# Optimization experiments

Measured on AMD Instinct MI355X. Metric: run time of the kernel, lower is better.

Reference implementation:

```python
import jax, jax.numpy as jnp
import numpy as np

B, NX, NY = 4, 128, 128
DIM, DH, HEADS, LATENT, DOUT = 128, 64, 8, 64, 128
KM = 3
KD = DH * KM          # per-head low-rank-kernel dim (192)
SCALING = 1.0         # kernel_multiplier<=4 and softmax=False -> scaling_factor
ROT_SCALE = 64.0      # 1/min_freq of continuous RotaryEmbedding (min_freq=1/64)
EPS = 1e-5


def layer_norm(x, g, b):
    m = x.mean(-1, keepdims=True)
    v = jnp.var(x, axis=-1, keepdims=True)
    return (x - m) * jax.lax.rsqrt(v + EPS) * g + b


def pooling_reducer(x, Win, g, b, W1, b1, W2, b2):
    # x: [b, n, m, c] -> mean over axis 2 -> PreNorm(MLP with gated GELU) -> [b, n, latent]
    h = (x @ Win).mean(axis=2)
    h = layer_norm(h, g, b)
    h = h @ W1 + b1
    c = h.shape[-1] // 2
    h = jax.nn.gelu(h[..., :c], approximate=False) * h[..., c:]
    return h @ W2 + b2


def rotary(t, pos):
    # t: [b,h,n,d], pos: [n] continuous coordinates
    d = t.shape[-1]
    inv_freq = 1.0 / (10000.0 ** (jnp.arange(0, d, 2, dtype=jnp.float32) / d))
    f = (pos * ROT_SCALE)[:, None] * inv_freq          # [n, d//2]
    f = jnp.concatenate([f, f], axis=-1)               # [n, d]
    cos, sin = jnp.cos(f), jnp.sin(f)
    x1, x2 = jnp.split(t, 2, axis=-1)
    rot = jnp.concatenate([-x2, x1], axis=-1)          # rotate_half (half-split variant)
    return t * cos + rot * sin


def low_rank_kernel(u, pos, Wqk):
    # u: [b, n, latent] -> kernel K: [b, h, n, n]
    b, n, _ = u.shape
    qk = u @ Wqk                                       # [b, n, 2*h*KD]
    q, k = jnp.split(qk, 2, axis=-1)
    q = q.reshape(b, n, HEADS, KD).transpose(0, 2, 1, 3)
    k = k.reshape(b, n, HEADS, KD).transpose(0, 2, 1, 3)
    q = rotary(q, pos)
    k = rotary(k, pos)
    return jnp.einsum('bhid,bhjd->bhij', q, k) * SCALING


def setup_inputs():
    key = jax.random.key(0)
    ks = jax.random.split(key, 16)
    s = 0.02
    def rn(k, shape):
        return jax.random.normal(k, shape, dtype=jnp.float32) * s
    return {
        'u': jax.random.normal(ks[0], (B, NX, NY, DIM), dtype=jnp.float32),
        'pos_x': jnp.sort(jax.random.uniform(ks[1], (NX,), dtype=jnp.float32)),
        'pos_y': jnp.sort(jax.random.uniform(ks[2], (NY,), dtype=jnp.float32)),
        'ln_g': jnp.ones((DIM,), jnp.float32),
        'ln_b': jnp.zeros((DIM,), jnp.float32),
        'Wv': rn(ks[3], (DIM, HEADS * DH)),
        'Win': rn(ks[4], (DIM, DIM)),
        'px_Win': rn(ks[5], (DIM, DIM)),
        'px_g': jnp.ones((DIM,), jnp.float32),
        'px_b': jnp.zeros((DIM,), jnp.float32),
        'px_W1': rn(ks[6], (DIM, 2 * DIM)),
        'px_b1': jnp.zeros((2 * DIM,), jnp.float32),
        'px_W2': rn(ks[7], (DIM, LATENT)),
        'px_b2': jnp.zeros((LATENT,), jnp.float32),
        'py_Win': rn(ks[8], (DIM, DIM)),
        'py_g': jnp.ones((DIM,), jnp.float32),
        'py_b': jnp.zeros((DIM,), jnp.float32),
        'py_W1': rn(ks[9], (DIM, 2 * DIM)),
        'py_b1': jnp.zeros((2 * DIM,), jnp.float32),
        'py_W2': rn(ks[10], (DIM, LATENT)),
        'py_b2': jnp.zeros((LATENT,), jnp.float32),
        'Wqk_x': rn(ks[11], (LATENT, 2 * HEADS * KD)),
        'Wqk_y': rn(ks[12], (LATENT, 2 * HEADS * KD)),
        'Wo1': rn(ks[13], (HEADS * DH, DOUT)),
        'Wo2': rn(ks[14], (DOUT, DOUT)),
    }


def reference(u, pos_x, pos_y, ln_g, ln_b, Wv, Win,
              px_Win, px_g, px_b, px_W1, px_b1, px_W2, px_b2,
              py_Win, py_g, py_b, py_W1, py_b1, py_W2, py_b2,
              Wqk_x, Wqk_y, Wo1, Wo2):
    un = layer_norm(u, ln_g, ln_b)                      # [b,nx,ny,dim]
    v = un @ Wv                                         # [b,nx,ny,h*dh]
    ui = un @ Win
    ux = pooling_reducer(ui, px_Win, px_g, px_b, px_W1, px_b1, px_W2, px_b2)                       # [b,nx,L]
    uy = pooling_reducer(ui.transpose(0, 2, 1, 3), py_Win, py_g, py_b, py_W1, py_b1, py_W2, py_b2)  # [b,ny,L]
    kx = low_rank_kernel(ux, pos_x, Wqk_x)              # [b,h,nx,nx]
    ky = low_rank_kernel(uy, pos_y, Wqk_y)              # [b,h,ny,ny]
    b, nx, ny, _ = u.shape
    vphi = v.reshape(b, nx, ny, HEADS, DH).transpose(0, 3, 1, 2, 4)   # b h i l c
    t = jnp.einsum('bhij,bhjmc->bhimc', kx, vphi)       # attend along x axis
    t = jnp.einsum('bhlm,bhimc->bhilc', ky, t)          # attend along y axis
    t = t.transpose(0, 2, 3, 1, 4).reshape(b, nx, ny, HEADS * DH)
    # InstanceNorm2d applied to a channels-LAST tensor (as in the original repo):
    # torch treats dim1 (nx) as channels, normalizing over (ny, h*dh) per (b, nx), no affine.
    m = t.mean(axis=(2, 3), keepdims=True)
    var = t.var(axis=(2, 3), keepdims=True)
    t = (t - m) * jax.lax.rsqrt(var + EPS)
    h = jax.nn.gelu(t @ Wo1, approximate=False)
    return h @ Wo2
```

## Files before the change

kernel.cpp:

```cpp
#include <hip/hip_runtime.h>
#include <math.h>

#define ROWS 65536
#define KDD 192

typedef __attribute__((ext_vector_type(8))) short bfrag;
typedef __attribute__((ext_vector_type(4))) float facc;

__device__ inline unsigned short bf16r(float x) {
  union { float f; unsigned u; } v; v.f = x;
  unsigned r = v.u + 0x7fffu + ((v.u >> 16) & 1u);
  return (unsigned short)(r >> 16);
}
__device__ inline float bf2f(unsigned short h) {
  union { unsigned u; float f; } v; v.u = ((unsigned)h) << 16; return v.f;
}
__device__ inline float gelu_f(float x) {
  return x * 0.5f * (1.f + erff(x * 0.70710678f));
}

__global__ __launch_bounds__(128) void k_ln(const float* __restrict__ x,
                                            const float* __restrict__ g,
                                            const float* __restrict__ bb,
                                            unsigned short* __restrict__ y) {
  int row = blockIdx.x;
  int t = threadIdx.x;
  float v = x[(size_t)row * 128 + t];
  float s = v, s2 = v * v;
  for (int off = 32; off > 0; off >>= 1) {
    s += __shfl_down(s, off, 64);
    s2 += __shfl_down(s2, off, 64);
  }
  __shared__ float ps[2], ps2[2];
  int wid = t >> 6, lane = t & 63;
  if (lane == 0) { ps[wid] = s; ps2[wid] = s2; }
  __syncthreads();
  float S = ps[0] + ps[1], S2 = ps2[0] + ps2[1];
  float mean = S * (1.f / 128.f);
  float var = S2 * (1.f / 128.f) - mean * mean;
  float r = rsqrtf(var + 1e-5f);
  y[(size_t)row * 128 + t] = bf16r((v - mean) * r * g[t] + bb[t]);
}

__global__ __launch_bounds__(128) void k_means(const unsigned short* __restrict__ un,
                                               float* __restrict__ mx, float* __restrict__ my) {
  int blk = blockIdx.x;
  int c = threadIdx.x;
  if (blk < 512) {
    const unsigned short* p = un + (size_t)blk * 16384 + c;
    float s = 0;
    for (int j = 0; j < 128; j++) s += bf2f(p[(size_t)j * 128]);
    mx[(size_t)blk * 128 + c] = s * (1.f / 128.f);
  } else {
    int bj = blk - 512;
    int b = bj >> 7, j = bj & 127;
    const unsigned short* p = un + (size_t)b * 2097152 + (size_t)j * 128 + c;
    float s = 0;
    for (int i = 0; i < 128; i++) s += bf2f(p[(size_t)i * 16384]);
    my[(size_t)bj * 128 + c] = s * (1.f / 128.f);
  }
}

__global__ __launch_bounds__(256) void k_wprep(const float* __restrict__ Wv,
                                               const float* __restrict__ Wo1,
                                               const float* __restrict__ Wo2,
                                               unsigned short* __restrict__ WvT,
                                               unsigned short* __restrict__ Wo1T,
                                               unsigned short* __restrict__ Wo2T,
                                               float* __restrict__ scol) {
  int blk = blockIdx.x, t = threadIdx.x;
  if (blk < 256) {
    int idx = blk * 256 + t;
    int c = idx >> 7, r = idx & 127;
    WvT[(size_t)c * 128 + r] = bf16r(Wv[(size_t)r * 512 + c]);
  } else if (blk < 512) {
    int idx = (blk - 256) * 256 + t;
    int n = idx >> 9, k = idx & 511;
    Wo1T[(size_t)n * 512 + k] = bf16r(Wo1[(size_t)k * 128 + n]);
  } else if (blk < 576) {
    int idx = (blk - 512) * 256 + t;
    int n = idx >> 7, k = idx & 127;
    Wo2T[n * 128 + k] = bf16r(Wo2[k * 128 + n]);
  } else {
    if (t < 128) {
      float a = 0;
      for (int k = 0; k < 512; k++) a += bf2f(bf16r(Wo1[k * 128 + t]));
      scol[t] = a;
    }
  }
}

__global__ __launch_bounds__(256) void k_gemmz(const float* __restrict__ A0,
                                               const float* __restrict__ B0,
                                               float* __restrict__ C0,
                                               const float* __restrict__ A1,
                                               const float* __restrict__ B1,
                                               float* __restrict__ C1,
                                               int K, int lda, int ldb, int ldc) {
  const float* A = blockIdx.z ? A1 : A0;
  const float* Bm = blockIdx.z ? B1 : B0;
  float* C = blockIdx.z ? C1 : C0;
  __shared__ float As[16][64];
  __shared__ float Bs[16][64];
  int tid = threadIdx.x;
  int n0 = blockIdx.x * 64, m0 = blockIdx.y * 64;
  int tx = tid & 15, ty = tid >> 4;
  float acc[4][4] = {};
  int la_m = tid >> 2, la_k = (tid & 3) * 4;
  int lb_k = tid >> 4, lb_n = (tid & 15) * 4;
  for (int k0 = 0; k0 < K; k0 += 16) {
    float4 a4 = *(const float4*)(A + (size_t)(m0 + la_m) * lda + k0 + la_k);
    As[la_k + 0][la_m] = a4.x; As[la_k + 1][la_m] = a4.y;
    As[la_k + 2][la_m] = a4.z; As[la_k + 3][la_m] = a4.w;
    float4 b4 = *(const float4*)(Bm + (size_t)(k0 + lb_k) * ldb + n0 + lb_n);
    *(float4*)&Bs[lb_k][lb_n] = b4;
    __syncthreads();
#pragma unroll
    for (int kk = 0; kk < 16; kk++) {
      float4 av = *(const float4*)&As[kk][ty * 4];
      float4 bv = *(const float4*)&Bs[kk][tx * 4];
      float a[4] = {av.x, av.y, av.z, av.w};
      float b[4] = {bv.x, bv.y, bv.z, bv.w};
#pragma unroll
      for (int i = 0; i < 4; i++)
#pragma unroll
        for (int j = 0; j < 4; j++) acc[i][j] += a[i] * b[j];
    }
    __syncthreads();
  }
#pragma unroll
  for (int i = 0; i < 4; i++) {
    float4 o;
    o.x = acc[i][0]; o.y = acc[i][1]; o.z = acc[i][2]; o.w = acc[i][3];
    *(float4*)(C + (size_t)(m0 + ty * 4 + i) * ldc + n0 + tx * 4) = o;
  }
}

__global__ __launch_bounds__(128) void k_pool2(const float* __restrict__ in0, const float* __restrict__ in1,
                                               const float* __restrict__ Wc0, const float* __restrict__ Wc1,
                                               const float* __restrict__ g0, const float* __restrict__ g1,
                                               const float* __restrict__ bb0, const float* __restrict__ bb1,
                                               const float* __restrict__ W10, const float* __restrict__ W11,
                                               const float* __restrict__ b10, const float* __restrict__ b11,
                                               const float* __restrict__ W20, const float* __restrict__ W21,
                                               const float* __restrict__ b20, const float* __restrict__ b21,
                                               float* __restrict__ o0, float* __restrict__ o1) {
  int sel = blockIdx.y;
  const float* in = sel ? in1 : in0;  const float* Wc = sel ? Wc1 : Wc0;
  const float* g = sel ? g1 : g0;     const float* bb = sel ? bb1 : bb0;
  const float* W1 = sel ? W11 : W10;  const float* b1 = sel ? b11 : b10;
  const float* W2 = sel ? W21 : W20;  const float* b2 = sel ? b21 : b20;
  float* out = sel ? o1 : o0;
  int row = blockIdx.x;
  int t = threadIdx.x;
  __shared__ float xin[128], h1[128], h3[128];
  __shared__ float ps[2], ps2[2];
  xin[t] = in[(size_t)row * 128 + t];
  __syncthreads();
  float a = 0;
  for (int k = 0; k < 128; k++) a += xin[k] * Wc[k * 128 + t];
  float s = a, s2 = a * a;
  for (int off = 32; off > 0; off >>= 1) {
    s += __shfl_down(s, off, 64);
    s2 += __shfl_down(s2, off, 64);
  }
  if ((t & 63) == 0) { ps[t >> 6] = s; ps2[t >> 6] = s2; }
  __syncthreads();
  float S = ps[0] + ps[1], S2 = ps2[0] + ps2[1];
  float mean = S * (1.f / 128.f);
  float var = S2 * (1.f / 128.f) - mean * mean;
  float r = rsqrtf(var + 1e-5f);
  h1[t] = (a - mean) * r * g[t] + bb[t];
  __syncthreads();
  float u1 = b1[t], u2 = b1[t + 128];
  for (int k = 0; k < 128; k++) {
    float hv = h1[k];
    u1 += hv * W1[k * 256 + t];
    u2 += hv * W1[k * 256 + t + 128];
  }
  h3[t] = gelu_f(u1) * u2;
  __syncthreads();
  if (t < 64) {
    float o = b2[t];
    for (int k = 0; k < 128; k++) o += h3[k] * W2[k * 64 + t];
    out[(size_t)row * 64 + t] = o;
  }
}

__global__ __launch_bounds__(192) void k_rot2(const float* __restrict__ qk0, const float* __restrict__ qk1,
                                              const float* __restrict__ pos0, const float* __restrict__ pos1,
                                              float* __restrict__ qr0, float* __restrict__ qr1,
                                              float* __restrict__ kr0, float* __restrict__ kr1) {
  int sel = blockIdx.y;
  const float* qk = sel ? qk1 : qk0;
  const float* pos = sel ? pos1 : pos0;
  float* qr = sel ? qr1 : qr0;
  float* kr = sel ? kr1 : kr0;
  int bn = blockIdx.x;
  int b = bn >> 7, n = bn & 127;
  int d = threadIdx.x;
  int fi = d % 96;
  float inv = expf(-logf(10000.f) * ((float)fi / 96.f));
  float f = pos[n] * 64.f * inv;
  float cs = cosf(f), sn = sinf(f);
  int partner = d < 96 ? d + 96 : d - 96;
  float sgn = d < 96 ? -1.f : 1.f;
  for (int h = 0; h < 8; h++) {
    float q = qk[(size_t)bn * 3072 + h * 192 + d];
    float qp = qk[(size_t)bn * 3072 + h * 192 + partner];
    float kx = qk[(size_t)bn * 3072 + 1536 + h * 192 + d];
    float kp = qk[(size_t)bn * 3072 + 1536 + h * 192 + partner];
    size_t o = ((size_t)(b * 8 + h) * 128 + n) * 192 + d;
    qr[o] = q * cs + sgn * qp * sn;
    kr[o] = kx * cs + sgn * kp * sn;
  }
}

__global__ __launch_bounds__(256) void k_qkt2(const float* __restrict__ Q0, const float* __restrict__ K0,
                                              unsigned short* __restrict__ C0,
                                              const float* __restrict__ Q1, const float* __restrict__ K1,
                                              unsigned short* __restrict__ C1) {
  int z = blockIdx.z;
  int bh = z & 31;
  const float* Qb = (z < 32 ? Q0 : Q1) + (size_t)bh * 128 * KDD;
  const float* Kb = (z < 32 ? K0 : K1) + (size_t)bh * 128 * KDD;
  unsigned short* Cb = (z < 32 ? C0 : C1) + (size_t)bh * 128 * 128;
  __shared__ float As[16][64];
  __shared__ float Bs[16][64];
  int tid = threadIdx.x;
  int i0 = blockIdx.y * 64, j0 = blockIdx.x * 64;
  int tx = tid & 15, ty = tid >> 4;
  float acc[4][4] = {};
  int l_m = tid >> 2, l_k = (tid & 3) * 4;
  for (int k0 = 0; k0 < KDD; k0 += 16) {
    float4 a4 = *(const float4*)(Qb + (size_t)(i0 + l_m) * KDD + k0 + l_k);
    As[l_k + 0][l_m] = a4.x; As[l_k + 1][l_m] = a4.y;
    As[l_k + 2][l_m] = a4.z; As[l_k + 3][l_m] = a4.w;
    float4 b4 = *(const float4*)(Kb + (size_t)(j0 + l_m) * KDD + k0 + l_k);
    Bs[l_k + 0][l_m] = b4.x; Bs[l_k + 1][l_m] = b4.y;
    Bs[l_k + 2][l_m] = b4.z; Bs[l_k + 3][l_m] = b4.w;
    __syncthreads();
#pragma unroll
    for (int kk = 0; kk < 16; kk++) {
      float4 av = *(const float4*)&As[kk][ty * 4];
      float4 bv = *(const float4*)&Bs[kk][tx * 4];
      float a[4] = {av.x, av.y, av.z, av.w};
      float b[4] = {bv.x, bv.y, bv.z, bv.w};
#pragma unroll
      for (int i = 0; i < 4; i++)
#pragma unroll
        for (int j = 0; j < 4; j++) acc[i][j] += a[i] * b[j];
    }
    __syncthreads();
  }
#pragma unroll
  for (int i = 0; i < 4; i++) {
    unsigned h0 = bf16r(acc[i][0]), h1 = bf16r(acc[i][1]);
    unsigned h2 = bf16r(acc[i][2]), h3 = bf16r(acc[i][3]);
    uint2 pk;
    pk.x = h0 | (h1 << 16);
    pk.y = h2 | (h3 << 16);
    *(uint2*)(Cb + (size_t)(i0 + ty * 4 + i) * 128 + j0 + tx * 4) = pk;
  }
}


__global__ __launch_bounds__(256) void k_vt(const unsigned short* __restrict__ WvT,
                                            const unsigned short* __restrict__ un,
                                            unsigned short* __restrict__ vT) {
  int nt = blockIdx.x;
  int mt = blockIdx.y;
  __shared__ __align__(16) unsigned short As[16384];
  __shared__ __align__(16) unsigned short Bs[16384];
  int tid = threadIdx.x;
  int w = tid >> 6, lane = tid & 63, quad = lane >> 4, l16 = lane & 15;
  {
    int r = tid >> 1, half = tid & 1;
    const unsigned short* sa = WvT + (size_t)(mt * 128 + r) * 128 + half * 64;
    const unsigned short* sbp = un + (size_t)(nt * 128 + r) * 128 + half * 64;
#pragma unroll
    for (int q = 0; q < 8; q++) {
      int c8 = half * 8 + q;
      int ph = ((c8 ^ (r & 15)) << 3);
      *(uint4*)&As[r * 128 + ph] = *(const uint4*)(sa + q * 8);
      *(uint4*)&Bs[r * 128 + ph] = *(const uint4*)(sbp + q * 8);
    }
  }
  __syncthreads();
  facc zf = {0.f, 0.f, 0.f, 0.f};
  facc acc[2][8];
#pragma unroll
  for (int a = 0; a < 2; a++)
#pragma unroll
    for (int bq = 0; bq < 8; bq++) acc[a][bq] = zf;
#pragma unroll
  for (int k0 = 0; k0 < 4; k0++) {
    bfrag av[2];
#pragma unroll
    for (int it = 0; it < 2; it++) {
      int row = (w + it * 4) * 16 + l16;
      av[it] = *(const bfrag*)&As[row * 128 + ((((k0 * 4 + quad) ^ l16)) << 3)];
    }
#pragma unroll
    for (int nt8 = 0; nt8 < 8; nt8++) {
      int row = nt8 * 16 + l16;
      bfrag bv = *(const bfrag*)&Bs[row * 128 + ((((k0 * 4 + quad) ^ l16)) << 3)];
      acc[0][nt8] = __builtin_amdgcn_mfma_f32_16x16x32_bf16(av[0], bv, acc[0][nt8], 0, 0, 0);
      acc[1][nt8] = __builtin_amdgcn_mfma_f32_16x16x32_bf16(av[1], bv, acc[1][nt8], 0, 0, 0);
    }
  }
  __syncthreads();
#pragma unroll
  for (int it = 0; it < 2; it++)
#pragma unroll
    for (int nt8 = 0; nt8 < 8; nt8++)
#pragma unroll
      for (int rr = 0; rr < 4; rr++) {
        int row = (w + it * 4) * 16 + quad * 4 + rr;
        int col = nt8 * 16 + l16;
        As[row * 128 + ((((col >> 3) ^ (row & 15)) << 3)) + (col & 7)] = bf16r(acc[it][nt8][rr]);
      }
  __syncthreads();
  {
    int r = tid >> 1, half = tid & 1;
    unsigned short* dst = vT + (size_t)(mt * 128 + r) * 65536 + (size_t)nt * 128 + half * 64;
#pragma unroll
    for (int q = 0; q < 8; q++) {
      int c8 = half * 8 + q;
      *(uint4*)(dst + q * 8) = *(const uint4*)&As[r * 128 + ((c8 ^ (r & 15)) << 3)];
    }
  }
}

__global__ __launch_bounds__(256) void k_fuse12(const unsigned short* __restrict__ kxall,
                                                const unsigned short* __restrict__ kyall,
                                                const unsigned short* __restrict__ vT,
                                                unsigned short* __restrict__ ttp,
                                                float* __restrict__ sb,
                                                float* __restrict__ s2b) {
  int blk = blockIdx.x;
  int bh = blk >> 4, strip = blk & 15;
  int b = bh >> 3, h = bh & 7;
  __shared__ __align__(16) unsigned short Ky[16384];
  __shared__ __align__(16) unsigned short Vs[16384];
  __shared__ float sL[128], s2L[128];
  int tid = threadIdx.x;
  int w = tid >> 6, lane = tid & 63, quad = lane >> 4, l16 = lane & 15;
  if (tid < 128) { sL[tid] = 0.f; s2L[tid] = 0.f; }
  {
    int r = tid >> 1, half = tid & 1;
    const unsigned short* s = kyall + (size_t)bh * 16384 + (size_t)r * 128 + half * 64;
#pragma unroll
    for (int q = 0; q < 8; q++) {
      int c8 = half * 8 + q;
      *(uint4*)&Ky[r * 128 + ((c8 ^ (r & 15)) << 3)] = *(const uint4*)(s + q * 8);
    }
  }
  uint4 axf[2][4];
#pragma unroll
  for (int it = 0; it < 2; it++) {
    int i = (w + it * 4) * 16 + l16;
#pragma unroll
    for (int k0 = 0; k0 < 4; k0++)
      axf[it][k0] = *(const uint4*)(kxall + (size_t)bh * 16384 + (size_t)i * 128 + k0 * 32 + quad * 8);
  }
  __syncthreads();
  facc zf = {0.f, 0.f, 0.f, 0.f};
  for (int cc = 0; cc < 4; cc++) {
    int c = strip * 4 + cc;
    if (cc) __syncthreads();
    {
      int r = tid >> 1, half = tid & 1;
      const unsigned short* s = vT + (size_t)(h * 64 + c) * 65536 + (size_t)b * 16384 +
                                (size_t)r * 128 + half * 64;
#pragma unroll
      for (int q = 0; q < 8; q++) {
        int c8 = half * 8 + q;
        *(uint4*)&Vs[r * 128 + ((c8 ^ (r & 15)) << 3)] = *(const uint4*)(s + q * 8);
      }
    }
    __syncthreads();
    facc a1[2][8];
#pragma unroll
    for (int a = 0; a < 2; a++)
#pragma unroll
      for (int bq = 0; bq < 8; bq++) a1[a][bq] = zf;
#pragma unroll
    for (int k0 = 0; k0 < 4; k0++) {
      bfrag av[2];
#pragma unroll
      for (int it = 0; it < 2; it++) {
        int row = (w + it * 4) * 16 + l16;
        av[it] = *(const bfrag*)&Vs[row * 128 + (((k0 * 4 + quad) ^ l16) << 3)];
      }
#pragma unroll
      for (int lt = 0; lt < 8; lt++) {
        int row = lt * 16 + l16;
        bfrag bv = *(const bfrag*)&Ky[row * 128 + (((k0 * 4 + quad) ^ l16) << 3)];
        a1[0][lt] = __builtin_amdgcn_mfma_f32_16x16x32_bf16(av[0], bv, a1[0][lt], 0, 0, 0);
        a1[1][lt] = __builtin_amdgcn_mfma_f32_16x16x32_bf16(av[1], bv, a1[1][lt], 0, 0, 0);
      }
    }
    __syncthreads();
#pragma unroll
    for (int it = 0; it < 2; it++)
#pragma unroll
      for (int lt = 0; lt < 8; lt++)
#pragma unroll
        for (int rr = 0; rr < 4; rr++) {
          int j = (w + it * 4) * 16 + quad * 4 + rr;
          int l = lt * 16 + l16;
          Vs[l * 128 + (((j >> 3) ^ (l & 15)) << 3) + (j & 7)] = bf16r(a1[it][lt][rr]);
        }
    __syncthreads();
    facc a2[2][8];
#pragma unroll
    for (int a = 0; a < 2; a++)
#pragma unroll
      for (int bq = 0; bq < 8; bq++) a2[a][bq] = zf;
#pragma unroll
    for (int k0 = 0; k0 < 4; k0++) {
      bfrag av0 = *(const bfrag*)&axf[0][k0];
      bfrag av1 = *(const bfrag*)&axf[1][k0];
#pragma unroll
      for (int lt = 0; lt < 8; lt++) {
        int row = lt * 16 + l16;
        bfrag bv = *(const bfrag*)&Vs[row * 128 + (((k0 * 4 + quad) ^ l16) << 3)];
        a2[0][lt] = __builtin_amdgcn_mfma_f32_16x16x32_bf16(av0, bv, a2[0][lt], 0, 0, 0);
        a2[1][lt] = __builtin_amdgcn_mfma_f32_16x16x32_bf16(av1, bv, a2[1][lt], 0, 0, 0);
      }
    }
    __syncthreads();
#pragma unroll
    for (int it = 0; it < 2; it++)
#pragma unroll
      for (int lt = 0; lt < 8; lt++)
#pragma unroll
        for (int rr = 0; rr < 4; rr++) {
          int i = (w + it * 4) * 16 + quad * 4 + rr;
          int l = lt * 16 + l16;
          Vs[i * 128 + (((l >> 3) ^ (i & 15)) << 3) + (l & 7)] = bf16r(a2[it][lt][rr]);
        }
    __syncthreads();
    {
      int r = tid >> 1, half = tid & 1;
      float s = 0.f, s2 = 0.f;
      unsigned short* dst = ttp + ((size_t)(bh * 64 + c) * 128 + r) * 128 + half * 64;
#pragma unroll
      for (int q = 0; q < 8; q++) {
        int c8 = half * 8 + q;
        uint4 v = *(const uint4*)&Vs[r * 128 + ((c8 ^ (r & 15)) << 3)];
        *(uint4*)(dst + q * 8) = v;
        unsigned short* pv = (unsigned short*)&v;
#pragma unroll
        for (int e = 0; e < 8; e++) { float f = bf2f(pv[e]); s += f; s2 += f * f; }
      }
      atomicAdd(&sL[r], s);
      atomicAdd(&s2L[r], s2);
    }
  }
  __syncthreads();
  if (tid < 128) {
    atomicAdd(&sb[b * 128 + tid], sL[tid]);
    atomicAdd(&s2b[b * 128 + tid], s2L[tid]);
  }
}

__global__ __launch_bounds__(256) void k_tail2(const unsigned short* __restrict__ ttp,
                                               const unsigned short* __restrict__ Wo1T,
                                               const unsigned short* __restrict__ Wo2T,
                                               float* __restrict__ out,
                                               const float* __restrict__ sb,
                                               const float* __restrict__ s2b,
                                               const float* __restrict__ sc) {
  int blk = blockIdx.x;
  int b = blk >> 7, i = blk & 127;
  __shared__ __align__(16) unsigned short As[16384];
  __shared__ __align__(16) unsigned short Bs[16384];
  int tid = threadIdx.x;
  int w = tid >> 6, lane = tid & 63, quad = lane >> 4, l16 = lane & 15;
  facc zf = {0.f, 0.f, 0.f, 0.f};
  facc a1[2][8];
#pragma unroll
  for (int a = 0; a < 2; a++)
#pragma unroll
    for (int bq = 0; bq < 8; bq++) a1[a][bq] = zf;
  for (int kc = 0; kc < 4; kc++) {
    if (kc) __syncthreads();
    {
      int r = tid >> 1, half = tid & 1;
      int hc = kc * 128 + r;
      const unsigned short* src = ttp + (((size_t)(b * 8 + (hc >> 6)) * 64 + (hc & 63)) * 128 + i) * 128 + half * 64;
#pragma unroll
      for (int q = 0; q < 8; q++) {
        uint4 v = *(const uint4*)(src + q * 8);
        unsigned short* pv = (unsigned short*)&v;
#pragma unroll
        for (int e = 0; e < 8; e++) {
          int l = half * 64 + q * 8 + e;
          As[l * 128 + (((r >> 3) ^ (l & 15)) << 3) + (r & 7)] = pv[e];
        }
      }
      const unsigned short* sB = Wo1T + (size_t)r * 512 + kc * 128 + half * 64;
#pragma unroll
      for (int q = 0; q < 8; q++) {
        int c8 = half * 8 + q;
        *(uint4*)&Bs[r * 128 + ((c8 ^ (r & 15)) << 3)] = *(const uint4*)(sB + q * 8);
      }
    }
    __syncthreads();
#pragma unroll
    for (int k0 = 0; k0 < 4; k0++) {
      bfrag av[2];
#pragma unroll
      for (int it = 0; it < 2; it++) {
        int row = (w + it * 4) * 16 + l16;
        av[it] = *(const bfrag*)&As[row * 128 + (((k0 * 4 + quad) ^ l16) << 3)];
      }
#pragma unroll
      for (int nt = 0; nt < 8; nt++) {
        int row = nt * 16 + l16;
        bfrag bv = *(const bfrag*)&Bs[row * 128 + (((k0 * 4 + quad) ^ l16) << 3)];
        a1[0][nt] = __builtin_amdgcn_mfma_f32_16x16x32_bf16(av[0], bv, a1[0][nt], 0, 0, 0);
        a1[1][nt] = __builtin_amdgcn_mfma_f32_16x16x32_bf16(av[1], bv, a1[1][nt], 0, 0, 0);
      }
    }
  }
  float S = sb[b * 128 + i], S2 = s2b[b * 128 + i];
  float mean = S * (1.f / 65536.f);
  float var = S2 * (1.f / 65536.f) - mean * mean;
  float rs = rsqrtf(var + 1e-5f);
  __syncthreads();
#pragma unroll
  for (int it = 0; it < 2; it++)
#pragma unroll
    for (int nt = 0; nt < 8; nt++) {
      int n1 = nt * 16 + l16;
      float scn = sc[n1];
#pragma unroll
      for (int rr = 0; rr < 4; rr++) {
        int l = (w + it * 4) * 16 + quad * 4 + rr;
        float val = (a1[it][nt][rr] - mean * scn) * rs;
        As[l * 128 + (((n1 >> 3) ^ (l & 15)) << 3) + (n1 & 7)] = bf16r(gelu_f(val));
      }
    }
  {
    int r = tid >> 1, half = tid & 1;
    const unsigned short* sB = Wo2T + (size_t)r * 128 + half * 64;
#pragma unroll
    for (int q = 0; q < 8; q++) {
      int c8 = half * 8 + q;
      *(uint4*)&Bs[r * 128 + ((c8 ^ (r & 15)) << 3)] = *(const uint4*)(sB + q * 8);
    }
  }
  __syncthreads();
  facc a2[2][8];
#pragma unroll
  for (int a = 0; a < 2; a++)
#pragma unroll
    for (int bq = 0; bq < 8; bq++) a2[a][bq] = zf;
#pragma unroll
  for (int k0 = 0; k0 < 4; k0++) {
    bfrag av[2];
#pragma unroll
    for (int it = 0; it < 2; it++) {
      int row = (w + it * 4) * 16 + l16;
      av[it] = *(const bfrag*)&As[row * 128 + (((k0 * 4 + quad) ^ l16) << 3)];
    }
#pragma unroll
    for (int nt = 0; nt < 8; nt++) {
      int row = nt * 16 + l16;
      bfrag bv = *(const bfrag*)&Bs[row * 128 + (((k0 * 4 + quad) ^ l16) << 3)];
      a2[0][nt] = __builtin_amdgcn_mfma_f32_16x16x32_bf16(av[0], bv, a2[0][nt], 0, 0, 0);
      a2[1][nt] = __builtin_amdgcn_mfma_f32_16x16x32_bf16(av[1], bv, a2[1][nt], 0, 0, 0);
    }
  }
#pragma unroll
  for (int it = 0; it < 2; it++)
#pragma unroll
    for (int nt = 0; nt < 8; nt++) {
      int n2 = nt * 16 + l16;
#pragma unroll
      for (int rr = 0; rr < 4; rr++) {
        int l = (w + it * 4) * 16 + quad * 4 + rr;
        out[((size_t)(b * 16384 + i * 128 + l)) * 128 + n2] = a2[it][nt][rr];
      }
    }
}

extern "C" void kernel_launch(void* const* d_in, const int* in_sizes, int n_in,
                              void* d_out, int out_size, void* d_ws, size_t ws_size,
                              hipStream_t stream) {
  const float* u = (const float*)d_in[0];
  const float* pos_x = (const float*)d_in[1];
  const float* pos_y = (const float*)d_in[2];
  const float* ln_g = (const float*)d_in[3];
  const float* ln_b = (const float*)d_in[4];
  const float* Wv = (const float*)d_in[5];
  const float* Win = (const float*)d_in[6];
  const float* px_Win = (const float*)d_in[7];
  const float* px_g = (const float*)d_in[8];
  const float* px_b = (const float*)d_in[9];
  const float* px_W1 = (const float*)d_in[10];
  const float* px_b1 = (const float*)d_in[11];
  const float* px_W2 = (const float*)d_in[12];
  const float* px_b2 = (const float*)d_in[13];
  const float* py_Win = (const float*)d_in[14];
  const float* py_g = (const float*)d_in[15];
  const float* py_b = (const float*)d_in[16];
  const float* py_W1 = (const float*)d_in[17];
  const float* py_b1 = (const float*)d_in[18];
  const float* py_W2 = (const float*)d_in[19];
  const float* py_b2 = (const float*)d_in[20];
  const float* Wqk_x = (const float*)d_in[21];
  const float* Wqk_y = (const float*)d_in[22];
  const float* Wo1 = (const float*)d_in[23];
  const float* Wo2 = (const float*)d_in[24];
  float* out = (float*)d_out;

  const size_t NEED = 44868736;
  if (ws_size < NEED * sizeof(float)) return;
  float* ws = (float*)d_ws;
  unsigned short* un_bf = (unsigned short*)ws;
  unsigned short* vT    = (unsigned short*)(ws + 4194304);
  unsigned short* ttp   = (unsigned short*)(ws + 20971520);
  float* small = ws + 37748736;
  float* mun_x = small;
  float* mun_y = small + 65536;
  float* Wcx   = small + 131072;
  float* Wcy   = small + 147456;
  float* ux    = small + 163840;
  float* uy    = small + 196608;
  float* qkx   = small + 229376;
  float* qky   = small + 1802240;
  float* qrx   = small + 3375104;
  float* krx   = small + 4161536;
  float* qry   = small + 4947968;
  float* kry   = small + 5734400;
  unsigned short* kx_bf = (unsigned short*)(small + 6520832);
  unsigned short* ky_bf = (unsigned short*)(small + 6782976);
  unsigned short* WvT   = (unsigned short*)(small + 7045120);
  unsigned short* Wo1T  = (unsigned short*)(small + 7077888);
  unsigned short* Wo2T  = (unsigned short*)(small + 7110656);
  float* sbuf  = small + 7118848;
  float* s2buf = small + 7119360;
  float* scol  = small + 7119872;

  hipMemsetAsync(sbuf, 0, 1024 * sizeof(float), stream);

  k_ln<<<ROWS, 128, 0, stream>>>(u, ln_g, ln_b, un_bf);
  k_means<<<1024, 128, 0, stream>>>(un_bf, mun_x, mun_y);
  k_wprep<<<577, 256, 0, stream>>>(Wv, Wo1, Wo2, WvT, Wo1T, Wo2T, scol);
  k_gemmz<<<dim3(2, 2, 2), 256, 0, stream>>>(Win, px_Win, Wcx, Win, py_Win, Wcy,
                                             128, 128, 128, 128);
  k_pool2<<<dim3(512, 2), 128, 0, stream>>>(mun_x, mun_y, Wcx, Wcy, px_g, py_g, px_b, py_b,
                                            px_W1, py_W1, px_b1, py_b1, px_W2, py_W2,
                                            px_b2, py_b2, ux, uy);
  k_gemmz<<<dim3(48, 8, 2), 256, 0, stream>>>(ux, Wqk_x, qkx, uy, Wqk_y, qky,
                                              64, 64, 3072, 3072);
  k_rot2<<<dim3(512, 2), 192, 0, stream>>>(qkx, qky, pos_x, pos_y, qrx, qry, krx, kry);
  k_qkt2<<<dim3(2, 2, 64), 256, 0, stream>>>(qrx, krx, kx_bf, qry, kry, ky_bf);

  k_vt<<<dim3(512, 4), 256, 0, stream>>>(WvT, un_bf, vT);
  k_fuse12<<<512, 256, 0, stream>>>(kx_bf, ky_bf, vT, ttp, sbuf, s2buf);
  k_tail2<<<512, 256, 0, stream>>>(ttp, Wo1T, Wo2T, out, sbuf, s2buf, scol);
}
```

Measured before the change: 349.9 us.

## Fuse rotary into QK^T, fold Win products into wprep, regrid vt and fuse12

Computes the rotary embedding inside the QK^T GEMM tile load, which removes the separate rotation kernel and its intermediate q/k buffers. The small Win x pooling-Win GEMMs move into the weight-prep kernel as extra blocks, saving one launch. k_vt now loops over the four output-channel tiles per block so the un tile is loaded once. k_fuse12 uses one block per channel (2048 blocks) instead of four channels per block, giving more parallelism and fewer barriers, but it reloads the Ky tile per channel and recomputes sin/cos in every QK tile.

```diff
diff --git a/kernel.cpp b/kernel.cpp
--- a/kernel.cpp
+++ b/kernel.cpp
@@ -64,10 +64,17 @@
 __global__ __launch_bounds__(256) void k_wprep(const float* __restrict__ Wv,
                                                const float* __restrict__ Wo1,
                                                const float* __restrict__ Wo2,
+                                               const float* __restrict__ Win,
+                                               const float* __restrict__ pxWin,
+                                               const float* __restrict__ pyWin,
                                                unsigned short* __restrict__ WvT,
                                                unsigned short* __restrict__ Wo1T,
                                                unsigned short* __restrict__ Wo2T,
+                                               float* __restrict__ Wcx,
+                                               float* __restrict__ Wcy,
                                                float* __restrict__ scol) {
+  __shared__ float As[16][64];
+  __shared__ float Bs[16][64];
   int blk = blockIdx.x, t = threadIdx.x;
   if (blk < 256) {
     int idx = blk * 256 + t;
@@ -81,11 +88,48 @@
     int idx = (blk - 512) * 256 + t;
     int n = idx >> 7, k = idx & 127;
     Wo2T[n * 128 + k] = bf16r(Wo2[k * 128 + n]);
-  } else {
+  } else if (blk == 576) {
     if (t < 128) {
       float a = 0;
       for (int k = 0; k < 512; k++) a += bf2f(bf16r(Wo1[k * 128 + t]));
       scol[t] = a;
+    }
+  } else {
+    int g = blk - 577;
+    int sel = g >> 2, t2 = g & 3;
+    const float* A = Win;
+    const float* Bm = sel ? pyWin : pxWin;
+    float* C = sel ? Wcy : Wcx;
+    int n0 = (t2 & 1) * 64, m0 = (t2 >> 1) * 64;
+    int tx = t & 15, ty = t >> 4;
+    float acc[4][4] = {};
+    int la_m = t >> 2, la_k = (t & 3) * 4;
+    int lb_k = t >> 4, lb_n = (t & 15) * 4;
+    for (int k0 = 0; k0 < 128; k0 += 16) {
+      float4 a4 = *(const float4*)(A + (size_t)(m0 + la_m) * 128 + k0 + la_k);
+      As[la_k + 0][la_m] = a4.x; As[la_k + 1][la_m] = a4.y;
+      As[la_k + 2][la_m] = a4.z; As[la_k + 3][la_m] = a4.w;
+      float4 b4 = *(const float4*)(Bm + (size_t)(k0 + lb_k) * 128 + n0 + lb_n);
+      *(float4*)&Bs[lb_k][lb_n] = b4;
+      __syncthreads();
+#pragma unroll
+      for (int kk = 0; kk < 16; kk++) {
+        float4 av = *(const float4*)&As[kk][ty * 4];
+        float4 bv = *(const float4*)&Bs[kk][tx * 4];
+        float a[4] = {av.x, av.y, av.z, av.w};
+        float b[4] = {bv.x, bv.y, bv.z, bv.w};
+#pragma unroll
+        for (int i = 0; i < 4; i++)
+#pragma unroll
+          for (int j = 0; j < 4; j++) acc[i][j] += a[i] * b[j];
+      }
+      __syncthreads();
+    }
+#pragma unroll
+    for (int i = 0; i < 4; i++) {
+      float4 o;
+      o.x = acc[i][0]; o.y = acc[i][1]; o.z = acc[i][2]; o.w = acc[i][3];
+      *(float4*)(C + (size_t)(m0 + ty * 4 + i) * 128 + n0 + tx * 4) = o;
     }
   }
 }
@@ -187,44 +231,18 @@
   }
 }
 
-__global__ __launch_bounds__(192) void k_rot2(const float* __restrict__ qk0, const float* __restrict__ qk1,
-                                              const float* __restrict__ pos0, const float* __restrict__ pos1,
-                                              float* __restrict__ qr0, float* __restrict__ qr1,
-                                              float* __restrict__ kr0, float* __restrict__ kr1) {
-  int sel = blockIdx.y;
-  const float* qk = sel ? qk1 : qk0;
-  const float* pos = sel ? pos1 : pos0;
-  float* qr = sel ? qr1 : qr0;
-  float* kr = sel ? kr1 : kr0;
-  int bn = blockIdx.x;
-  int b = bn >> 7, n = bn & 127;
-  int d = threadIdx.x;
-  int fi = d % 96;
-  float inv = expf(-logf(10000.f) * ((float)fi / 96.f));
-  float f = pos[n] * 64.f * inv;
-  float cs = cosf(f), sn = sinf(f);
-  int partner = d < 96 ? d + 96 : d - 96;
-  float sgn = d < 96 ? -1.f : 1.f;
-  for (int h = 0; h < 8; h++) {
-    float q = qk[(size_t)bn * 3072 + h * 192 + d];
-    float qp = qk[(size_t)bn * 3072 + h * 192 + partner];
-    float kx = qk[(size_t)bn * 3072 + 1536 + h * 192 + d];
-    float kp = qk[(size_t)bn * 3072 + 1536 + h * 192 + partner];
-    size_t o = ((size_t)(b * 8 + h) * 128 + n) * 192 + d;
-    qr[o] = q * cs + sgn * qp * sn;
-    kr[o] = kx * cs + sgn * kp * sn;
-  }
-}
-
-__global__ __launch_bounds__(256) void k_qkt2(const float* __restrict__ Q0, const float* __restrict__ K0,
-                                              unsigned short* __restrict__ C0,
-                                              const float* __restrict__ Q1, const float* __restrict__ K1,
-                                              unsigned short* __restrict__ C1) {
+__global__ __launch_bounds__(256) void k_qkt3(const float* __restrict__ qkx,
+                                              const float* __restrict__ qky,
+                                              const float* __restrict__ pos_x,
+                                              const float* __restrict__ pos_y,
+                                              unsigned short* __restrict__ Cx,
+                                              unsigned short* __restrict__ Cy) {
   int z = blockIdx.z;
   int bh = z & 31;
-  const float* Qb = (z < 32 ? Q0 : Q1) + (size_t)bh * 128 * KDD;
-  const float* Kb = (z < 32 ? K0 : K1) + (size_t)bh * 128 * KDD;
-  unsigned short* Cb = (z < 32 ? C0 : C1) + (size_t)bh * 128 * 128;
+  int b = bh >> 3, h = bh & 7;
+  const float* qk = (z < 32) ? qkx : qky;
+  const float* pos = (z < 32) ? pos_x : pos_y;
+  unsigned short* Cb = ((z < 32) ? Cx : Cy) + (size_t)bh * 16384;
   __shared__ float As[16][64];
   __shared__ float Bs[16][64];
   int tid = threadIdx.x;
@@ -232,24 +250,58 @@
   int tx = tid & 15, ty = tid >> 4;
   float acc[4][4] = {};
   int l_m = tid >> 2, l_k = (tid & 3) * 4;
+  const float LOG1E4 = 9.21034037f;
   for (int k0 = 0; k0 < KDD; k0 += 16) {
-    float4 a4 = *(const float4*)(Qb + (size_t)(i0 + l_m) * KDD + k0 + l_k);
-    As[l_k + 0][l_m] = a4.x; As[l_k + 1][l_m] = a4.y;
-    As[l_k + 2][l_m] = a4.z; As[l_k + 3][l_m] = a4.w;
-    float4 b4 = *(const float4*)(Kb + (size_t)(j0 + l_m) * KDD + k0 + l_k);
-    Bs[l_k + 0][l_m] = b4.x; Bs[l_k + 1][l_m] = b4.y;
-    Bs[l_k + 2][l_m] = b4.z; Bs[l_k + 3][l_m] = b4.w;
+    int d = k0 + l_k;
+    int fi = d % 96;
+    int prt = d < 96 ? d + 96 : d - 96;
+    float sgn = d < 96 ? -1.f : 1.f;
+    float cs[4], sn[4];
+    {
+      int nA = i0 + l_m;
+      float p64 = pos[nA] * 64.f;
+#pragma unroll
+      for (int q = 0; q < 4; q++) {
+        float inv = expf(-LOG1E4 * ((float)(fi + q) * (1.f / 96.f)));
+        float f = p64 * inv;
+        cs[q] = cosf(f); sn[q] = sinf(f);
+      }
+      const float* base = qk + (size_t)(b * 128 + nA) * 3072 + h * 192;
+      float4 tq = *(const float4*)(base + d);
+      float4 tp = *(const float4*)(base + prt);
+      As[l_k + 0][l_m] = tq.x * cs[0] + sgn * tp.x * sn[0];
+      As[l_k + 1][l_m] = tq.y * cs[1] + sgn * tp.y * sn[1];
+      As[l_k + 2][l_m] = tq.z * cs[2] + sgn * tp.z * sn[2];
+      As[l_k + 3][l_m] = tq.w * cs[3] + sgn * tp.w * sn[3];
+    }
+    {
+      int nB = j0 + l_m;
+      float p64 = pos[nB] * 64.f;
+#pragma unroll
+      for (int q = 0; q < 4; q++) {
+        float inv = expf(-LOG1E4 * ((float)(fi + q) * (1.f / 96.f)));
+        float f = p64 * inv;
+        cs[q] = cosf(f); sn[q] = sinf(f);
+      }
+      const float* base = qk + (size_t)(b * 128 + nB) * 3072 + 1536 + h * 192;
+      float4 tq = *(const float4*)(base + d);
+      float4 tp = *(const float4*)(base + prt);
+      Bs[l_k + 0][l_m] = tq.x * cs[0] + sgn * tp.x * sn[0];
+      Bs[l_k + 1][l_m] = tq.y * cs[1] + sgn * tp.y * sn[1];
+      Bs[l_k + 2][l_m] = tq.z * cs[2] + sgn * tp.z * sn[2];
+      Bs[l_k + 3][l_m] = tq.w * cs[3] + sgn * tp.w * sn[3];
+    }
     __syncthreads();
 #pragma unroll
     for (int kk = 0; kk < 16; kk++) {
       float4 av = *(const float4*)&As[kk][ty * 4];
       float4 bv = *(const float4*)&Bs[kk][tx * 4];
       float a[4] = {av.x, av.y, av.z, av.w};
-      float b[4] = {bv.x, bv.y, bv.z, bv.w};
+      float bb[4] = {bv.x, bv.y, bv.z, bv.w};
 #pragma unroll
       for (int i = 0; i < 4; i++)
 #pragma unroll
-        for (int j = 0; j < 4; j++) acc[i][j] += a[i] * b[j];
+        for (int j = 0; j < 4; j++) acc[i][j] += a[i] * bb[j];
     }
     __syncthreads();
   }
@@ -269,65 +321,73 @@
                                             const unsigned short* __restrict__ un,
                                             unsigned short* __restrict__ vT) {
   int nt = blockIdx.x;
-  int mt = blockIdx.y;
   __shared__ __align__(16) unsigned short As[16384];
   __shared__ __align__(16) unsigned short Bs[16384];
   int tid = threadIdx.x;
   int w = tid >> 6, lane = tid & 63, quad = lane >> 4, l16 = lane & 15;
   {
     int r = tid >> 1, half = tid & 1;
-    const unsigned short* sa = WvT + (size_t)(mt * 128 + r) * 128 + half * 64;
     const unsigned short* sbp = un + (size_t)(nt * 128 + r) * 128 + half * 64;
 #pragma unroll
     for (int q = 0; q < 8; q++) {
       int c8 = half * 8 + q;
-      int ph = ((c8 ^ (r & 15)) << 3);
-      *(uint4*)&As[r * 128 + ph] = *(const uint4*)(sa + q * 8);
-      *(uint4*)&Bs[r * 128 + ph] = *(const uint4*)(sbp + q * 8);
-    }
-  }
-  __syncthreads();
+      *(uint4*)&Bs[r * 128 + ((c8 ^ (r & 15)) << 3)] = *(const uint4*)(sbp + q * 8);
+    }
+  }
   facc zf = {0.f, 0.f, 0.f, 0.f};
-  facc acc[2][8];
-#pragma unroll
-  for (int a = 0; a < 2; a++)
-#pragma unroll
-    for (int bq = 0; bq < 8; bq++) acc[a][bq] = zf;
-#pragma unroll
-  for (int k0 = 0; k0 < 4; k0++) {
-    bfrag av[2];
-#pragma unroll
-    for (int it = 0; it < 2; it++) {
-      int row = (w + it * 4) * 16 + l16;
-      av[it] = *(const bfrag*)&As[row * 128 + ((((k0 * 4 + quad) ^ l16)) << 3)];
-    }
-#pragma unroll
-    for (int nt8 = 0; nt8 < 8; nt8++) {
-      int row = nt8 * 16 + l16;
-      bfrag bv = *(const bfrag*)&Bs[row * 128 + ((((k0 * 4 + quad) ^ l16)) << 3)];
-      acc[0][nt8] = __builtin_amdgcn_mfma_f32_16x16x32_bf16(av[0], bv, acc[0][nt8], 0, 0, 0);
-      acc[1][nt8] = __builtin_amdgcn_mfma_f32_16x16x32_bf16(av[1], bv, acc[1][nt8], 0, 0, 0);
-    }
-  }
-  __syncthreads();
-#pragma unroll
-  for (int it = 0; it < 2; it++)
-#pragma unroll
-    for (int nt8 = 0; nt8 < 8; nt8++)
-#pragma unroll
-      for (int rr = 0; rr < 4; rr++) {
-        int row = (w + it * 4) * 16 + quad * 4 + rr;
-        int col = nt8 * 16 + l16;
-        As[row * 128 + ((((col >> 3) ^ (row & 15)) << 3)) + (col & 7)] = bf16r(acc[it][nt8][rr]);
-      }
-  __syncthreads();
-  {
-    int r = tid >> 1, half = tid & 1;
-    unsigned short* dst = vT + (size_t)(mt * 128 + r) * 65536 + (size_t)nt * 128 + half * 64;
-#pragma unroll
-    for (int q = 0; q < 8; q++) {
-      int c8 = half * 8 + q;
-      *(uint4*)(dst + q * 8) = *(const uint4*)&As[r * 128 + ((c8 ^ (r & 15)) << 3)];
+  for (int mt = 0; mt < 4; mt++) {
+    if (mt) __syncthreads();
+    {
+      int r = tid >> 1, half = tid & 1;
+      const unsigned short* sa = WvT + (size_t)(mt * 128 + r) * 128 + half * 64;
+#pragma unroll
+      for (int q = 0; q < 8; q++) {
+        int c8 = half * 8 + q;
+        *(uint4*)&As[r * 128 + ((c8 ^ (r & 15)) << 3)] = *(const uint4*)(sa + q * 8);
+      }
+    }
+    __syncthreads();
+    facc acc[2][8];
+#pragma unroll
+    for (int a = 0; a < 2; a++)
+#pragma unroll
+      for (int bq = 0; bq < 8; bq++) acc[a][bq] = zf;
+#pragma unroll
+    for (int k0 = 0; k0 < 4; k0++) {
+      bfrag av[2];
+#pragma unroll
+      for (int it = 0; it < 2; it++) {
+        int row = (w + it * 4) * 16 + l16;
+        av[it] = *(const bfrag*)&As[row * 128 + (((k0 * 4 + quad) ^ l16) << 3)];
+      }
+#pragma unroll
+      for (int nt8 = 0; nt8 < 8; nt8++) {
+        int row = nt8 * 16 + l16;
+        bfrag bv = *(const bfrag*)&Bs[row * 128 + (((k0 * 4 + quad) ^ l16) << 3)];
+        acc[0][nt8] = __builtin_amdgcn_mfma_f32_16x16x32_bf16(av[0], bv, acc[0][nt8], 0, 0, 0);
+        acc[1][nt8] = __builtin_amdgcn_mfma_f32_16x16x32_bf16(av[1], bv, acc[1][nt8], 0, 0, 0);
+      }
+    }
+    __syncthreads();
+#pragma unroll
+    for (int it = 0; it < 2; it++)
+#pragma unroll
+      for (int nt8 = 0; nt8 < 8; nt8++)
+#pragma unroll
+        for (int rr = 0; rr < 4; rr++) {
+          int row = (w + it * 4) * 16 + quad * 4 + rr;
+          int col = nt8 * 16 + l16;
+          As[row * 128 + (((col >> 3) ^ (row & 15)) << 3) + (col & 7)] = bf16r(acc[it][nt8][rr]);
+        }
+    __syncthreads();
+    {
+      int r = tid >> 1, half = tid & 1;
+      unsigned short* dst = vT + (size_t)(mt * 128 + r) * 65536 + (size_t)nt * 128 + half * 64;
+#pragma unroll
+      for (int q = 0; q < 8; q++) {
+        int c8 = half * 8 + q;
+        *(uint4*)(dst + q * 8) = *(const uint4*)&As[r * 128 + ((c8 ^ (r & 15)) << 3)];
+      }
     }
   }
 }
@@ -339,7 +399,7 @@
                                                 float* __restrict__ sb,
                                                 float* __restrict__ s2b) {
   int blk = blockIdx.x;
-  int bh = blk >> 4, strip = blk & 15;
+  int bh = blk >> 6, c = blk & 63;
   int b = bh >> 3, h = bh & 7;
   __shared__ __align__(16) unsigned short Ky[16384];
   __shared__ __align__(16) unsigned short Vs[16384];
@@ -350,10 +410,14 @@
   {
     int r = tid >> 1, half = tid & 1;
     const unsigned short* s = kyall + (size_t)bh * 16384 + (size_t)r * 128 + half * 64;
+    const unsigned short* sv = vT + (size_t)(h * 64 + c) * 65536 + (size_t)b * 16384 +
+                               (size_t)r * 128 + half * 64;
 #pragma unroll
     for (int q = 0; q < 8; q++) {
       int c8 = half * 8 + q;
-      *(uint4*)&Ky[r * 128 + ((c8 ^ (r & 15)) << 3)] = *(const uint4*)(s + q * 8);
+      int ph = ((c8 ^ (r & 15)) << 3);
+      *(uint4*)&Ky[r * 128 + ph] = *(const uint4*)(s + q * 8);
+      *(uint4*)&Vs[r * 128 + ph] = *(const uint4*)(sv + q * 8);
     }
   }
   uint4 axf[2][4];
@@ -366,98 +430,82 @@
   }
   __syncthreads();
   facc zf = {0.f, 0.f, 0.f, 0.f};
-  for (int cc = 0; cc < 4; cc++) {
-    int c = strip * 4 + cc;
-    if (cc) __syncthreads();
-    {
-      int r = tid >> 1, half = tid & 1;
-      const unsigned short* s = vT + (size_t)(h * 64 + c) * 65536 + (size_t)b * 16384 +
-                                (size_t)r * 128 + half * 64;
-#pragma unroll
-      for (int q = 0; q < 8; q++) {
-        int c8 = half * 8 + q;
-        *(uint4*)&Vs[r * 128 + ((c8 ^ (r & 15)) << 3)] = *(const uint4*)(s + q * 8);
-      }
-    }
-    __syncthreads();
-    facc a1[2][8];
-#pragma unroll
-    for (int a = 0; a < 2; a++)
-#pragma unroll
-      for (int bq = 0; bq < 8; bq++) a1[a][bq] = zf;
-#pragma unroll
-    for (int k0 = 0; k0 < 4; k0++) {
-      bfrag av[2];
-#pragma unroll
-      for (int it = 0; it < 2; it++) {
-        int row = (w + it * 4) * 16 + l16;
-        av[it] = *(const bfrag*)&Vs[row * 128 + (((k0 * 4 + quad) ^ l16) << 3)];
-      }
-#pragma unroll
-      for (int lt = 0; lt < 8; lt++) {
-        int row = lt * 16 + l16;
-        bfrag bv = *(const bfrag*)&Ky[row * 128 + (((k0 * 4 + quad) ^ l16) << 3)];
-        a1[0][lt] = __builtin_amdgcn_mfma_f32_16x16x32_bf16(av[0], bv, a1[0][lt], 0, 0, 0);
-        a1[1][lt] = __builtin_amdgcn_mfma_f32_16x16x32_bf16(av[1], bv, a1[1][lt], 0, 0, 0);
-      }
-    }
-    __syncthreads();
-#pragma unroll
-    for (int it = 0; it < 2; it++)
-#pragma unroll
-      for (int lt = 0; lt < 8; lt++)
-#pragma unroll
-        for (int rr = 0; rr < 4; rr++) {
-          int j = (w + it * 4) * 16 + quad * 4 + rr;
-          int l = lt * 16 + l16;
-          Vs[l * 128 + (((j >> 3) ^ (l & 15)) << 3) + (j & 7)] = bf16r(a1[it][lt][rr]);
-        }
-    __syncthreads();
-    facc a2[2][8];
-#pragma unroll
-    for (int a = 0; a < 2; a++)
-#pragma unroll
-      for (int bq = 0; bq < 8; bq++) a2[a][bq] = zf;
-#pragma unroll
-    for (int k0 = 0; k0 < 4; k0++) {
-      bfrag av0 = *(const bfrag*)&axf[0][k0];
-      bfrag av1 = *(const bfrag*)&axf[1][k0];
-#pragma unroll
-      for (int lt = 0; lt < 8; lt++) {
-        int row = lt * 16 + l16;
-        bfrag bv = *(const bfrag*)&Vs[row * 128 + (((k0 * 4 + quad) ^ l16) << 3)];
-        a2[0][lt] = __builtin_amdgcn_mfma_f32_16x16x32_bf16(av0, bv, a2[0][lt], 0, 0, 0);
-        a2[1][lt] = __builtin_amdgcn_mfma_f32_16x16x32_bf16(av1, bv, a2[1][lt], 0, 0, 0);
-      }
-    }
-    __syncthreads();
-#pragma unroll
-    for (int it = 0; it < 2; it++)
-#pragma unroll
-      for (int lt = 0; lt < 8; lt++)
-#pragma unroll
-        for (int rr = 0; rr < 4; rr++) {
-          int i = (w + it * 4) * 16 + quad * 4 + rr;
-          int l = lt * 16 + l16;
-          Vs[i * 128 + (((l >> 3) ^ (i & 15)) << 3) + (l & 7)] = bf16r(a2[it][lt][rr]);
-        }
-    __syncthreads();
-    {
-      int r = tid >> 1, half = tid & 1;
-      float s = 0.f, s2 = 0.f;
-      unsigned short* dst = ttp + ((size_t)(bh * 64 + c) * 128 + r) * 128 + half * 64;
-#pragma unroll
-      for (int q = 0; q < 8; q++) {
-        int c8 = half * 8 + q;
-        uint4 v = *(const uint4*)&Vs[r * 128 + ((c8 ^ (r & 15)) << 3)];
-        *(uint4*)(dst + q * 8) = v;
-        unsigned short* pv = (unsigned short*)&v;
-#pragma unroll
-        for (int e = 0; e < 8; e++) { float f = bf2f(pv[e]); s += f; s2 += f * f; }
-      }
-      atomicAdd(&sL[r], s);
-      atomicAdd(&s2L[r], s2);
-    }
+  facc a1[2][8];
+#pragma unroll
+  for (int a = 0; a < 2; a++)
+#pragma unroll
+    for (int bq = 0; bq < 8; bq++) a1[a][bq] = zf;
+#pragma unroll
+  for (int k0 = 0; k0 < 4; k0++) {
+    bfrag av[2];
+#pragma unroll
+    for (int it = 0; it < 2; it++) {
+      int row = (w + it * 4) * 16 + l16;
+      av[it] = *(const bfrag*)&Vs[row * 128 + (((k0 * 4 + quad) ^ l16) << 3)];
+    }
+#pragma unroll
+    for (int lt = 0; lt < 8; lt++) {
+      int row = lt * 16 + l16;
+      bfrag bv = *(const bfrag*)&Ky[row * 128 + (((k0 * 4 + quad) ^ l16) << 3)];
+      a1[0][lt] = __builtin_amdgcn_mfma_f32_16x16x32_bf16(av[0], bv, a1[0][lt], 0, 0, 0);
+      a1[1][lt] = __builtin_amdgcn_mfma_f32_16x16x32_bf16(av[1], bv, a1[1][lt], 0, 0, 0);
+    }
+  }
+  __syncthreads();
+#pragma unroll
+  for (int it = 0; it < 2; it++)
+#pragma unroll
+    for (int lt = 0; lt < 8; lt++)
+#pragma unroll
+      for (int rr = 0; rr < 4; rr++) {
+        int j = (w + it * 4) * 16 + quad * 4 + rr;
+        int l = lt * 16 + l16;
+        Ky[l * 128 + (((j >> 3) ^ (l & 15)) << 3) + (j & 7)] = bf16r(a1[it][lt][rr]);
+      }
+  __syncthreads();
+  facc a2[2][8];
+#pragma unroll
+  for (int a = 0; a < 2; a++)
+#pragma unroll
+    for (int bq = 0; bq < 8; bq++) a2[a][bq] = zf;
+#pragma unroll
+  for (int k0 = 0; k0 < 4; k0++) {
+    bfrag av0 = *(const bfrag*)&axf[0][k0];
+    bfrag av1 = *(const bfrag*)&axf[1][k0];
+#pragma unroll
+    for (int lt = 0; lt < 8; lt++) {
+      int row = lt * 16 + l16;
+      bfrag bv = *(const bfrag*)&Ky[row * 128 + (((k0 * 4 + quad) ^ l16) << 3)];
+      a2[0][lt] = __builtin_amdgcn_mfma_f32_16x16x32_bf16(av0, bv, a2[0][lt], 0, 0, 0);
+      a2[1][lt] = __builtin_amdgcn_mfma_f32_16x16x32_bf16(av1, bv, a2[1][lt], 0, 0, 0);
+    }
+  }
+#pragma unroll
+  for (int it = 0; it < 2; it++)
+#pragma unroll
+    for (int lt = 0; lt < 8; lt++)
+#pragma unroll
+      for (int rr = 0; rr < 4; rr++) {
+        int i = (w + it * 4) * 16 + quad * 4 + rr;
+        int l = lt * 16 + l16;
+        Vs[i * 128 + (((l >> 3) ^ (i & 15)) << 3) + (l & 7)] = bf16r(a2[it][lt][rr]);
+      }
+  __syncthreads();
+  {
+    int r = tid >> 1, half = tid & 1;
+    float s = 0.f, s2 = 0.f;
+    unsigned short* dst = ttp + ((size_t)(bh * 64 + c) * 128 + r) * 128 + half * 64;
+#pragma unroll
+    for (int q = 0; q < 8; q++) {
+      int c8 = half * 8 + q;
+      uint4 v = *(const uint4*)&Vs[r * 128 + ((c8 ^ (r & 15)) << 3)];
+      *(uint4*)(dst + q * 8) = v;
+      unsigned short* pv = (unsigned short*)&v;
+#pragma unroll
+      for (int e = 0; e < 8; e++) { float f = bf2f(pv[e]); s += f; s2 += f * f; }
+    }
+    atomicAdd(&sL[r], s);
+    atomicAdd(&s2L[r], s2);
   }
   __syncthreads();
   if (tid < 128) {
@@ -618,7 +666,7 @@
   const float* Wo2 = (const float*)d_in[24];
   float* out = (float*)d_out;
 
-  const size_t NEED = 44868736;
+  const size_t NEED = 41723008;
   if (ws_size < NEED * sizeof(float)) return;
   float* ws = (float*)d_ws;
   unsigned short* un_bf = (unsigned short*)ws;
@@ -633,35 +681,29 @@
   float* uy    = small + 196608;
   float* qkx   = small + 229376;
   float* qky   = small + 1802240;
-  float* qrx   = small + 3375104;
-  float* krx   = small + 4161536;
-  float* qry   = small + 4947968;
-  float* kry   = small + 5734400;
-  unsigned short* kx_bf = (unsigned short*)(small + 6520832);
-  unsigned short* ky_bf = (unsigned short*)(small + 6782976);
-  unsigned short* WvT   = (unsigned short*)(small + 7045120);
-  unsigned short* Wo1T  = (unsigned short*)(small + 7077888);
-  unsigned short* Wo2T  = (unsigned short*)(small + 7110656);
-  float* sbuf  = small + 7118848;
-  float* s2buf = small + 7119360;
-  float* scol  = small + 7119872;
+  unsigned short* kx_bf = (unsigned short*)(small + 3375104);
+  unsigned short* ky_bf = (unsigned short*)(small + 3637248);
+  unsigned short* WvT   = (unsigned short*)(small + 3899392);
+  unsigned short* Wo1T  = (unsigned short*)(small + 3932160);
+  unsigned short* Wo2T  = (unsigned short*)(small + 3964928);
+  float* sbuf  = small + 3973120;
+  float* s2buf = small + 3973632;
+  float* scol  = small + 3974144;
 
   hipMemsetAsync(sbuf, 0, 1024 * sizeof(float), stream);
 
   k_ln<<<ROWS, 128, 0, stream>>>(u, ln_g, ln_b, un_bf);
   k_means<<<1024, 128, 0, stream>>>(un_bf, mun_x, mun_y);
-  k_wprep<<<577, 256, 0, stream>>>(Wv, Wo1, Wo2, WvT, Wo1T, Wo2T, scol);
-  k_gemmz<<<dim3(2, 2, 2), 256, 0, stream>>>(Win, px_Win, Wcx, Win, py_Win, Wcy,
-                                             128, 128, 128, 128);
+  k_wprep<<<585, 256, 0, stream>>>(Wv, Wo1, Wo2, Win, px_Win, py_Win,
+                                   WvT, Wo1T, Wo2T, Wcx, Wcy, scol);
   k_pool2<<<dim3(512, 2), 128, 0, stream>>>(mun_x, mun_y, Wcx, Wcy, px_g, py_g, px_b, py_b,
                                             px_W1, py_W1, px_b1, py_b1, px_W2, py_W2,
                                             px_b2, py_b2, ux, uy);
   k_gemmz<<<dim3(48, 8, 2), 256, 0, stream>>>(ux, Wqk_x, qkx, uy, Wqk_y, qky,
                                               64, 64, 3072, 3072);
-  k_rot2<<<dim3(512, 2), 192, 0, stream>>>(qkx, qky, pos_x, pos_y, qrx, qry, krx, kry);
-  k_qkt2<<<dim3(2, 2, 64), 256, 0, stream>>>(qrx, krx, kx_bf, qry, kry, ky_bf);
-
-  k_vt<<<dim3(512, 4), 256, 0, stream>>>(WvT, un_bf, vT);
-  k_fuse12<<<512, 256, 0, stream>>>(kx_bf, ky_bf, vT, ttp, sbuf, s2buf);
+  k_qkt3<<<dim3(2, 2, 64), 256, 0, stream>>>(qkx, qky, pos_x, pos_y, kx_bf, ky_bf);
+
+  k_vt<<<512, 256, 0, stream>>>(WvT, un_bf, vT);
+  k_fuse12<<<2048, 256, 0, stream>>>(kx_bf, ky_bf, vT, ttp, sbuf, s2buf);
   k_tail2<<<512, 256, 0, stream>>>(ttp, Wo1T, Wo2T, out, sbuf, s2buf, scol);
 }
```

Result: slower. 357.0 us (+2.0%).
